# Performance work log

Hardware: AMD Instinct MI355X
Metric: run time of the kernel (lower is better)

Reference implementation:

```python
import jax, jax.numpy as jnp
import numpy as np

N, D, K = 65536, 512, 4096


def setup_inputs() -> dict:
    key = jax.random.key(0)
    kx, kc = jax.random.split(key)
    x = jax.random.normal(kx, (N, D), dtype=jnp.float32)
    center = jax.random.normal(kc, (K, D), dtype=jnp.float32)
    return {"x": x, "center": center}


def squared_euclidean(x, center):
    x_sq = jnp.sum(x * x, axis=1, keepdims=True)        # [N,1]
    c_sq = jnp.sum(center * center, axis=1)             # [K]
    cross = x @ center.T                                # [N,K] GEMM
    return x_sq - 2.0 * cross + c_sq[None, :]


def reference(x, center):
    # KMeans.forward: dis_func(input, center).argmin(1)
    dist = squared_euclidean(x, center)                 # [N,K]
    return jnp.argmin(dist, axis=1)                     # [N] int32
```

## Files before the change

### kernel.cpp

```cpp
#include <hip/hip_runtime.h>

#define N_ROWS 65536
#define DIM    512
#define K_CENT 4096
#define TILE_M 128
#define TILE_N 128
#define BK     64
#define KSTEPS (DIM / BK)
#define NKT    (K_CENT / TILE_N)
#define THREADS 512
#define MARGIN 22.0f
#define CAND_CAP 1536
#define COMPACT_TRIG 1024
#define SCALE1 0x7F7F7F7F

typedef float  floatx4  __attribute__((ext_vector_type(4)));
typedef float  floatx16 __attribute__((ext_vector_type(16)));
typedef int    intx2    __attribute__((ext_vector_type(2)));
typedef int    intx4    __attribute__((ext_vector_type(4)));
typedef int    intx8    __attribute__((ext_vector_type(8)));

__device__ __forceinline__ unsigned mapF(float f) {
  unsigned u = __float_as_uint(f);
  return (u & 0x80000000u) ? ~u : (u | 0x80000000u);
}
__device__ __forceinline__ float unmapF(unsigned m) {
  unsigned u = (m & 0x80000000u) ? (m ^ 0x80000000u) : ~m;
  return __uint_as_float(u);
}

__device__ __forceinline__ void gload_lds16(const void* g, void* l) {
  __builtin_amdgcn_global_load_lds(
      (const __attribute__((address_space(1))) void*)g,
      (__attribute__((address_space(3))) void*)l, 16, 0, 0);
}

__device__ __forceinline__ int pk4(float a, float b, float c, float d) {
  int r = __builtin_amdgcn_cvt_pk_fp8_f32(a, b, 0, false);
  r = __builtin_amdgcn_cvt_pk_fp8_f32(c, d, r, true);
  return r;
}

#define FENCE_BAR() do { asm volatile("s_waitcnt lgkmcnt(0)" ::: "memory"); \
                         __builtin_amdgcn_s_barrier();                       \
                         __builtin_amdgcn_sched_barrier(0); } while (0)

__global__ void prep_convert(const float* __restrict__ c,
                             unsigned char* __restrict__ cq, float* __restrict__ csqg) {
  size_t i = ((size_t)blockIdx.x * blockDim.x + threadIdx.x) * 16;
  if (i >= (size_t)K_CENT * DIM) return;
  floatx4 a0 = *(const floatx4*)(c + i);
  floatx4 a1 = *(const floatx4*)(c + i + 4);
  floatx4 a2 = *(const floatx4*)(c + i + 8);
  floatx4 a3 = *(const floatx4*)(c + i + 12);
  intx4 q = { pk4(a0[0],a0[1],a0[2],a0[3]), pk4(a1[0],a1[1],a1[2],a1[3]),
              pk4(a2[0],a2[1],a2[2],a2[3]), pk4(a3[0],a3[1],a3[2],a3[3]) };
  *(intx4*)(cq + i) = q;
  float s = 0.f;
#pragma unroll
  for (int e = 0; e < 4; ++e)
    s += a0[e]*a0[e] + a1[e]*a1[e] + a2[e]*a2[e] + a3[e]*a3[e];
#pragma unroll
  for (int o = 1; o < 32; o <<= 1) s += __shfl_xor(s, o, 64);
  if ((threadIdx.x & 31) == 0) csqg[i >> 9] = s;
}

__global__ __launch_bounds__(THREADS, 4)
void kmeans_argmin_pipe(const float* __restrict__ x, const float* __restrict__ cent,
                        const unsigned char* __restrict__ cq,
                        const float* __restrict__ csqg, int* __restrict__ out) {
  extern __shared__ __align__(16) unsigned char dynLds[];
  __shared__ float csqL[K_CENT];
  __shared__ unsigned sminU[TILE_M];
  __shared__ unsigned long long best[TILE_M];
  __shared__ unsigned candKey[CAND_CAP];
  __shared__ float candS[CAND_CAP];
  __shared__ int candCount;

  const int t = threadIdx.x;
  const int lane = t & 63;
  const int wave = t >> 6;
  const int wm = wave >> 1;
  const int wn = wave & 1;
  const int l31 = lane & 31;
  const int half = lane >> 5;
  const int rowBlock = blockIdx.x * TILE_M;
  const int srow = wm * 32 + l31;

  if (t < TILE_M) { sminU[t] = 0xFFFFFFFFu; best[t] = ~0ull; }
  if (t == 0) candCount = 0;
#pragma unroll
  for (int i = 0; i < K_CENT / THREADS; ++i) {
    int idx = t + i * THREADS;
    csqL[idx] = csqg[idx];
  }

  const int rS = (t >> 2) & 31;
  const int rowS = (t >> 7) * 32 + rS;
  const int offS = (((t & 3) ^ ((rS >> 1) & 3)) << 4);
  unsigned bOff = (unsigned)(rowS * DIM + offS);

  const int qk = half * 2;
  const int fragSlotBase = 4 * l31 + (qk ^ ((l31 >> 1) & 3));
  const unsigned char* pB0  = dynLds + (((wn * 2 + 0) * 128 + fragSlotBase) * 16);
  const unsigned char* pB0x = dynLds + ((((wn * 2 + 0) * 128 + fragSlotBase) ^ 1) * 16);
  const unsigned char* pB1  = dynLds + (((wn * 2 + 1) * 128 + fragSlotBase) * 16);
  const unsigned char* pB1x = dynLds + ((((wn * 2 + 1) * 128 + fragSlotBase) ^ 1) * 16);

  intx8 xf[KSTEPS];
  {
    const float* xr = x + (size_t)(rowBlock + srow) * DIM + half * 32;
#pragma unroll
    for (int ks = 0; ks < KSTEPS; ++ks) {
      int q[8];
#pragma unroll
      for (int j = 0; j < 8; ++j) {
        floatx4 f = *(const floatx4*)(xr + ks * 64 + j * 4);
        q[j] = pk4(f[0], f[1], f[2], f[3]);
      }
      xf[ks] = (intx8){q[0], q[1], q[2], q[3], q[4], q[5], q[6], q[7]};
    }
  }

  asm volatile("s_waitcnt vmcnt(0)" ::: "memory");
  gload_lds16(cq + bOff, dynLds + 0 * 8192 + wave * 1024); bOff += 64;
  gload_lds16(cq + bOff, dynLds + 1 * 8192 + wave * 1024); bOff += 64;
  FENCE_BAR();

  for (int kt = 0; kt < NKT; ++kt) {
    floatx16 acc[2];
#pragma unroll
    for (int fn = 0; fn < 2; ++fn)
#pragma unroll
      for (int e = 0; e < 16; ++e) acc[fn][e] = 0.f;

#pragma unroll
    for (int p = 0; p < KSTEPS; ++p) {
      gload_lds16(cq + bOff, dynLds + (((p + 2) & 3) << 13) + wave * 1024);
      bOff += (p == 5) ? (65536 - 7 * 64) : 64;
      asm volatile("s_waitcnt vmcnt(2)" ::: "memory");
      __builtin_amdgcn_s_barrier();
      __builtin_amdgcn_sched_barrier(0);

      const int bo = (p & 3) << 13;
      intx4 lo0 = *(const intx4*)(pB0  + bo);
      intx4 hi0 = *(const intx4*)(pB0x + bo);
      intx4 lo1 = *(const intx4*)(pB1  + bo);
      intx4 hi1 = *(const intx4*)(pB1x + bo);
      asm volatile("s_waitcnt lgkmcnt(0)" ::: "memory");
      __builtin_amdgcn_sched_barrier(0);
      intx8 b0 = (intx8){lo0[0], lo0[1], lo0[2], lo0[3], hi0[0], hi0[1], hi0[2], hi0[3]};
      intx8 b1 = (intx8){lo1[0], lo1[1], lo1[2], lo1[3], hi1[0], hi1[1], hi1[2], hi1[3]};
      acc[0] = __builtin_amdgcn_mfma_scale_f32_32x32x64_f8f6f4(
          b0, xf[p], acc[0], 0, 0, 0, SCALE1, 0, SCALE1);
      acc[1] = __builtin_amdgcn_mfma_scale_f32_32x32x64_f8f6f4(
          b1, xf[p], acc[1], 0, 0, 0, SCALE1, 0, SCALE1);
    }

    const int ktBase = kt << 7;
    float mn = 3.4e38f;
#pragma unroll
    for (int fn = 0; fn < 2; ++fn)
#pragma unroll
      for (int g = 0; g < 4; ++g) {
        floatx4 cs4 = *(const floatx4*)&csqL[ktBase + (wn * 2 + fn) * 32 + 8 * g + 4 * half];
#pragma unroll
        for (int e = 0; e < 4; ++e)
          mn = fminf(mn, cs4[e] - 2.f * acc[fn][4 * g + e]);
      }
    mn = fminf(mn, __shfl_xor(mn, 32, 64));
    if (half == 0) atomicMin(&sminU[srow], mapF(mn));
    FENCE_BAR();

    {
      float thr = unmapF(sminU[srow]) + MARGIN;
#pragma unroll
      for (int fn = 0; fn < 2; ++fn)
#pragma unroll
        for (int g = 0; g < 4; ++g) {
          floatx4 cs4 = *(const floatx4*)&csqL[ktBase + (wn * 2 + fn) * 32 + 8 * g + 4 * half];
#pragma unroll
          for (int e = 0; e < 4; ++e) {
            float s = cs4[e] - 2.f * acc[fn][4 * g + e];
            if (s <= thr) {
              int k = ktBase + (wn * 2 + fn) * 32 + 8 * g + 4 * half + e;
              int idx = atomicAdd(&candCount, 1);
              if (idx < CAND_CAP) {
                candKey[idx] = ((unsigned)k << 7) | (unsigned)srow;
                candS[idx] = s;
              }
            }
          }
        }
    }
    FENCE_BAR();

    if (candCount > COMPACT_TRIG) {
      int cc = candCount; if (cc > CAND_CAP) cc = CAND_CAP;
      unsigned myK[4]; float myS[4]; int myN = 0;
      for (int i = t; i < cc; i += THREADS) {
        int rl = candKey[i] & 127;
        if (candS[i] <= unmapF(sminU[rl]) + MARGIN && myN < 4) {
          myK[myN] = candKey[i]; myS[myN] = candS[i]; ++myN;
        }
      }
      FENCE_BAR();
      if (t == 0) candCount = 0;
      FENCE_BAR();
      int base = atomicAdd(&candCount, myN);
      for (int jj = 0; jj < myN; ++jj) { candKey[base + jj] = myK[jj]; candS[base + jj] = myS[jj]; }
      FENCE_BAR();
    }
  }

  __syncthreads();

  int cnt = candCount; if (cnt > CAND_CAP) cnt = CAND_CAP;
  const int g = t >> 4;
  const int sl = t & 15;
  for (int ci = g; ci < cnt; ci += 32) {
    unsigned cd = candKey[ci];
    int rl = cd & 127;
    if (candS[ci] > unmapF(sminU[rl]) + MARGIN) continue;
    int k = cd >> 7;
    const float* xr = x + (size_t)(rowBlock + rl) * DIM;
    const float* cr = cent + (size_t)k * DIM;
    double d = 0.0;
#pragma unroll
    for (int jj = 0; jj < DIM / 64; ++jj) {
      floatx4 xv = *(const floatx4*)(xr + jj * 64 + sl * 4);
      floatx4 cv = *(const floatx4*)(cr + jj * 64 + sl * 4);
#pragma unroll
      for (int e = 0; e < 4; ++e) {
        double df = (double)xv[e] - (double)cv[e];
        d += df * df;
      }
    }
#pragma unroll
    for (int off = 1; off < 16; off <<= 1) d += __shfl_xor(d, off, 64);
    if (sl == 0) {
      unsigned long long key =
          ((unsigned long long)__double_as_longlong(d) & ~0xFFFull) | (unsigned long long)k;
      atomicMin(&best[rl], key);
    }
  }
  __syncthreads();
  if (t < TILE_M) out[rowBlock + t] = (int)(best[t] & 0xFFFull);
}

__global__ __launch_bounds__(THREADS, 4)
void kmeans_argmin_fb(const float* __restrict__ x, const float* __restrict__ cent,
                      int* __restrict__ out) {
  __shared__ unsigned char ldsA[TILE_M * BK];
  __shared__ unsigned char ldsB[TILE_N * BK];
  __shared__ float csq4[TILE_N][4];
  __shared__ unsigned sminU[TILE_M];
  __shared__ unsigned long long best[TILE_M];
  __shared__ unsigned candKey[CAND_CAP];
  __shared__ float candS[CAND_CAP];
  __shared__ int candCount;

  const int t = threadIdx.x;
  const int lane = t & 63;
  const int wave = t >> 6;
  const int wm = wave >> 1;
  const int wn = wave & 1;
  const int l31 = lane & 31;
  const int half = lane >> 5;
  const int rowBlock = blockIdx.x * TILE_M;

  if (t < TILE_M) { sminU[t] = 0xFFFFFFFFu; best[t] = ~0ull; }
  if (t == 0) candCount = 0;

  const int rS = (t >> 2) & 31;
  const int rowS = (t >> 7) * 32 + rS;
  const int offS = (((t & 3) ^ ((rS >> 1) & 3)) << 4);
  const int qk = half * 2;
  const int fragSlotBase = 4 * l31 + (qk ^ ((l31 >> 1) & 3));

  for (int kt = 0; kt < NKT; ++kt) {
    const int ktBase = kt * TILE_N;
    ((float*)csq4)[t] = 0.f;
    floatx16 acc[2];
#pragma unroll
    for (int fn = 0; fn < 2; ++fn)
#pragma unroll
      for (int e = 0; e < 16; ++e) acc[fn][e] = 0.f;

    for (int ks = 0; ks < KSTEPS; ++ks) {
      const int kd = ks * BK;
      {
        const float* gA = x + (size_t)(rowBlock + rowS) * DIM + kd + offS;
        floatx4 f0 = *(const floatx4*)gA, f1 = *(const floatx4*)(gA + 4);
        floatx4 f2 = *(const floatx4*)(gA + 8), f3 = *(const floatx4*)(gA + 12);
        intx4 q = { pk4(f0[0],f0[1],f0[2],f0[3]), pk4(f1[0],f1[1],f1[2],f1[3]),
                    pk4(f2[0],f2[1],f2[2],f2[3]), pk4(f3[0],f3[1],f3[2],f3[3]) };
        *(intx4*)(ldsA + (size_t)t * 16) = q;
      }
      {
        const float* gB = cent + (size_t)(ktBase + rowS) * DIM + kd + offS;
        floatx4 f0 = *(const floatx4*)gB, f1 = *(const floatx4*)(gB + 4);
        floatx4 f2 = *(const floatx4*)(gB + 8), f3 = *(const floatx4*)(gB + 12);
        intx4 q = { pk4(f0[0],f0[1],f0[2],f0[3]), pk4(f1[0],f1[1],f1[2],f1[3]),
                    pk4(f2[0],f2[1],f2[2],f2[3]), pk4(f3[0],f3[1],f3[2],f3[3]) };
        *(intx4*)(ldsB + (size_t)t * 16) = q;
        float s = 0.f;
#pragma unroll
        for (int e = 0; e < 4; ++e)
          s += f0[e]*f0[e] + f1[e]*f1[e] + f2[e]*f2[e] + f3[e]*f3[e];
        csq4[rowS][t & 3] += s;
      }
      __syncthreads();

      intx8 aF, bF[2];
      {
        int s0 = wm * 128 + fragSlotBase;
        intx4 lo = *(const intx4*)(ldsA + s0 * 16);
        intx4 hi = *(const intx4*)(ldsA + (s0 ^ 1) * 16);
        aF = (intx8){lo[0], lo[1], lo[2], lo[3], hi[0], hi[1], hi[2], hi[3]};
      }
#pragma unroll
      for (int fn = 0; fn < 2; ++fn) {
        int s0 = (wn * 2 + fn) * 128 + fragSlotBase;
        intx4 lo = *(const intx4*)(ldsB + s0 * 16);
        intx4 hi = *(const intx4*)(ldsB + (s0 ^ 1) * 16);
        bF[fn] = (intx8){lo[0], lo[1], lo[2], lo[3], hi[0], hi[1], hi[2], hi[3]};
      }
#pragma unroll
      for (int fn = 0; fn < 2; ++fn)
        acc[fn] = __builtin_amdgcn_mfma_scale_f32_32x32x64_f8f6f4(
            aF, bF[fn], acc[fn], 0, 0, 0, SCALE1, 0, SCALE1);
      __syncthreads();
    }

    float cs[2];
#pragma unroll
    for (int fn = 0; fn < 2; ++fn) {
      int cl = wn * 64 + fn * 32 + l31;
      cs[fn] = csq4[cl][0] + csq4[cl][1] + csq4[cl][2] + csq4[cl][3];
    }

#pragma unroll
    for (int r = 0; r < 16; ++r) {
      float v = fminf(cs[0] - 2.f * acc[0][r], cs[1] - 2.f * acc[1][r]);
      v = fminf(v, __shfl_xor(v, 1, 64));
      v = fminf(v, __shfl_xor(v, 2, 64));
      v = fminf(v, __shfl_xor(v, 4, 64));
      v = fminf(v, __shfl_xor(v, 8, 64));
      v = fminf(v, __shfl_xor(v, 16, 64));
      if (l31 == 0) {
        int srow = wm * 32 + (r & 3) + 8 * (r >> 2) + 4 * half;
        atomicMin(&sminU[srow], mapF(v));
      }
    }
    __syncthreads();

#pragma unroll
    for (int r = 0; r < 16; ++r) {
      int srow = wm * 32 + (r & 3) + 8 * (r >> 2) + 4 * half;
      float thr = unmapF(sminU[srow]) + MARGIN;
#pragma unroll
      for (int fn = 0; fn < 2; ++fn) {
        float s = cs[fn] - 2.f * acc[fn][r];
        if (s <= thr) {
          int k = ktBase + wn * 64 + fn * 32 + l31;
          int idx = atomicAdd(&candCount, 1);
          if (idx < CAND_CAP) {
            candKey[idx] = ((unsigned)k << 7) | (unsigned)srow;
            candS[idx] = s;
          }
        }
      }
    }
    __syncthreads();

    if (candCount > COMPACT_TRIG) {
      int cc = candCount; if (cc > CAND_CAP) cc = CAND_CAP;
      unsigned myK[4]; float myS[4]; int myN = 0;
      for (int i = t; i < cc; i += THREADS) {
        int rl = candKey[i] & 127;
        if (candS[i] <= unmapF(sminU[rl]) + MARGIN && myN < 4) {
          myK[myN] = candKey[i]; myS[myN] = candS[i]; ++myN;
        }
      }
      __syncthreads();
      if (t == 0) candCount = 0;
      __syncthreads();
      int base = atomicAdd(&candCount, myN);
      for (int j = 0; j < myN; ++j) { candKey[base + j] = myK[j]; candS[base + j] = myS[j]; }
      __syncthreads();
    }
  }

  int cnt = candCount; if (cnt > CAND_CAP) cnt = CAND_CAP;
  const int g = t >> 4;
  const int sl = t & 15;
  for (int ci = g; ci < cnt; ci += 32) {
    unsigned cd = candKey[ci];
    int rl = cd & 127;
    if (candS[ci] > unmapF(sminU[rl]) + MARGIN) continue;
    int k = cd >> 7;
    const float* xr = x + (size_t)(rowBlock + rl) * DIM;
    const float* cr = cent + (size_t)k * DIM;
    double d = 0.0;
#pragma unroll
    for (int j = 0; j < DIM / 64; ++j) {
      floatx4 xv = *(const floatx4*)(xr + j * 64 + sl * 4);
      floatx4 cv = *(const floatx4*)(cr + j * 64 + sl * 4);
#pragma unroll
      for (int e = 0; e < 4; ++e) {
        double df = (double)xv[e] - (double)cv[e];
        d += df * df;
      }
    }
#pragma unroll
    for (int off = 1; off < 16; off <<= 1) d += __shfl_xor(d, off, 64);
    if (sl == 0) {
      unsigned long long key =
          ((unsigned long long)__double_as_longlong(d) & ~0xFFFull) | (unsigned long long)k;
      atomicMin(&best[rl], key);
    }
  }
  __syncthreads();
  if (t < TILE_M) out[rowBlock + t] = (int)(best[t] & 0xFFFull);
}

extern "C" void kernel_launch(void* const* d_in, const int* in_sizes, int n_in,
                              void* d_out, int out_size, void* d_ws, size_t ws_size,
                              hipStream_t stream) {
  const float* x = (const float*)d_in[0];
  const float* cent = (const float*)d_in[1];
  int* out = (int*)d_out;
  const size_t nXq = (size_t)N_ROWS * DIM;
  const size_t nCq = (size_t)K_CENT * DIM;
  const size_t nCsq = (size_t)K_CENT * sizeof(float);
  const int grid = N_ROWS / TILE_M;

  if (ws_size >= nXq + nCq + nCsq) {
    unsigned char* cq = (unsigned char*)d_ws;
    float* csqg = (float*)(cq + nCq);
    const size_t total16 = nCq / 16;
    prep_convert<<<(unsigned)((total16 + 255) / 256), 256, 0, stream>>>(cent, cq, csqg);
    kmeans_argmin_pipe<<<grid, THREADS, 4 * 8192, stream>>>(x, cent, cq, csqg, out);
  } else {
    kmeans_argmin_fb<<<grid, THREADS, 0, stream>>>(x, cent, out);
  }
}
```

Baseline: 601.9 us.

## Give each wave a private centroid ring and 64 rows to drop block barriers

Restructures the main kernel so each of four waves owns 64 x-rows, kept as FP8 fragments in registers, and streams its own copy of each 64-centroid tile through a per-wave 4-slot LDS ring. This removes the per-k-step block-wide barriers and gives each B fragment reuse across two A fragments. Candidate pools and their compaction also become per-wave, so only wave-local fences are needed. The cost is four times the centroid traffic per block, much higher register and LDS use, and one block per CU via launch bounds, which lowers occupancy.

After: 605.8 us. Within noise of the previous version (+0.6%).

```diff
diff --git a/kernel.cpp b/kernel.cpp
--- a/kernel.cpp
+++ b/kernel.cpp
@@ -3,20 +3,18 @@
 #define N_ROWS 65536
 #define DIM    512
 #define K_CENT 4096
-#define TILE_M 128
-#define TILE_N 128
-#define BK     64
-#define KSTEPS (DIM / BK)
-#define NKT    (K_CENT / TILE_N)
-#define THREADS 512
+#define TILE_M 256
+#define TILE_N 64
+#define NCT    (K_CENT / TILE_N)
+#define KSTEPS 8
+#define THREADS 256
+#define WCAP   1024
+#define WTRIG  512
 #define MARGIN 22.0f
-#define CAND_CAP 1536
-#define COMPACT_TRIG 1024
 #define SCALE1 0x7F7F7F7F
 
 typedef float  floatx4  __attribute__((ext_vector_type(4)));
 typedef float  floatx16 __attribute__((ext_vector_type(16)));
-typedef int    intx2    __attribute__((ext_vector_type(2)));
 typedef int    intx4    __attribute__((ext_vector_type(4)));
 typedef int    intx8    __attribute__((ext_vector_type(8)));
 
@@ -41,9 +39,8 @@
   return r;
 }
 
-#define FENCE_BAR() do { asm volatile("s_waitcnt lgkmcnt(0)" ::: "memory"); \
-                         __builtin_amdgcn_s_barrier();                       \
-                         __builtin_amdgcn_sched_barrier(0); } while (0)
+#define WAVE_LDS_FENCE() do { asm volatile("s_waitcnt lgkmcnt(0)" ::: "memory"); \
+                              __builtin_amdgcn_sched_barrier(0); } while (0)
 
 __global__ void prep_convert(const float* __restrict__ c,
                              unsigned char* __restrict__ cq, float* __restrict__ csqg) {
@@ -65,16 +62,238 @@
   if ((threadIdx.x & 31) == 0) csqg[i >> 9] = s;
 }
 
-__global__ __launch_bounds__(THREADS, 4)
+__global__ __launch_bounds__(THREADS, 1)
 void kmeans_argmin_pipe(const float* __restrict__ x, const float* __restrict__ cent,
                         const unsigned char* __restrict__ cq,
                         const float* __restrict__ csqg, int* __restrict__ out) {
-  extern __shared__ __align__(16) unsigned char dynLds[];
-  __shared__ float csqL[K_CENT];
+  __shared__ __align__(16) unsigned char ringLds[4][16384];
+  __shared__ __align__(16) float csqL[K_CENT];
   __shared__ unsigned sminU[TILE_M];
   __shared__ unsigned long long best[TILE_M];
-  __shared__ unsigned candKey[CAND_CAP];
-  __shared__ float candS[CAND_CAP];
+  __shared__ unsigned poolK[4][WCAP];
+  __shared__ float    poolS[4][WCAP];
+  __shared__ int candCnt[4];
+
+  const int t = threadIdx.x;
+  const int lane = t & 63;
+  const int wave = t >> 6;
+  const int l31 = lane & 31;
+  const int half = lane >> 5;
+  const int rowBlock = blockIdx.x * TILE_M;
+
+  sminU[t] = 0xFFFFFFFFu;
+  best[t] = ~0ull;
+  if (t < 4) candCnt[t] = 0;
+#pragma unroll
+  for (int i = 0; i < K_CENT / THREADS; ++i) csqL[t + i * THREADS] = csqg[t + i * THREADS];
+
+  int offI0, offI1, offI2, offI3;
+#pragma unroll
+  for (int i = 0; i < 4; ++i) {
+    int s = i * 64 + lane;
+    int rS = (s >> 2) & 31;
+    int row = (s >> 7) * 32 + rS;
+    int cp = (s & 3) ^ ((rS >> 1) & 3);
+    int v = row * DIM + cp * 16;
+    if (i == 0) offI0 = v; else if (i == 1) offI1 = v;
+    else if (i == 2) offI2 = v; else offI3 = v;
+  }
+
+  const int qk = half * 2;
+  const int slotLo = 4 * l31 + (qk ^ ((l31 >> 1) & 3));
+  const int loB = slotLo * 16;
+  const int hiB = (slotLo ^ 1) * 16;
+  unsigned char* ringW = ringLds[wave];
+
+  intx8 xfA[KSTEPS], xfB[KSTEPS];
+  {
+    const float* xr = x + (size_t)(rowBlock + wave * 64 + l31) * DIM + half * 32;
+#pragma unroll
+    for (int ks = 0; ks < KSTEPS; ++ks) {
+      int q[8];
+#pragma unroll
+      for (int j = 0; j < 8; ++j) {
+        floatx4 f = *(const floatx4*)(xr + ks * 64 + j * 4);
+        q[j] = pk4(f[0], f[1], f[2], f[3]);
+      }
+      xfA[ks] = (intx8){q[0], q[1], q[2], q[3], q[4], q[5], q[6], q[7]};
+    }
+    xr += (size_t)32 * DIM;
+#pragma unroll
+    for (int ks = 0; ks < KSTEPS; ++ks) {
+      int q[8];
+#pragma unroll
+      for (int j = 0; j < 8; ++j) {
+        floatx4 f = *(const floatx4*)(xr + ks * 64 + j * 4);
+        q[j] = pk4(f[0], f[1], f[2], f[3]);
+      }
+      xfB[ks] = (intx8){q[0], q[1], q[2], q[3], q[4], q[5], q[6], q[7]};
+    }
+  }
+
+  __syncthreads();
+
+#pragma unroll
+  for (int s = 0; s < 3; ++s) {
+    unsigned char* wb = ringW + (s << 12);
+    gload_lds16(cq + s * 64 + offI0, wb);
+    gload_lds16(cq + s * 64 + offI1, wb + 1024);
+    gload_lds16(cq + s * 64 + offI2, wb + 2048);
+    gload_lds16(cq + s * 64 + offI3, wb + 3072);
+  }
+  unsigned sOff = 3 * 64;
+
+  for (int ct = 0; ct < NCT; ++ct) {
+    floatx16 acc00, acc01, acc10, acc11;
+#pragma unroll
+    for (int e = 0; e < 16; ++e) { acc00[e] = 0.f; acc01[e] = 0.f; acc10[e] = 0.f; acc11[e] = 0.f; }
+
+#pragma unroll
+    for (int p = 0; p < KSTEPS; ++p) {
+      {
+        unsigned char* wb = ringW + (((p + 3) & 3) << 12);
+        gload_lds16(cq + sOff + offI0, wb);
+        gload_lds16(cq + sOff + offI1, wb + 1024);
+        gload_lds16(cq + sOff + offI2, wb + 2048);
+        gload_lds16(cq + sOff + offI3, wb + 3072);
+      }
+      sOff += (p == 4) ? 32320u : 64u;
+      asm volatile("s_waitcnt vmcnt(12)" ::: "memory");
+      __builtin_amdgcn_sched_barrier(0);
+
+      const unsigned char* rb = ringW + ((p & 3) << 12);
+      intx4 lo0 = *(const intx4*)(rb + loB);
+      intx4 hi0 = *(const intx4*)(rb + hiB);
+      intx4 lo1 = *(const intx4*)(rb + 2048 + loB);
+      intx4 hi1 = *(const intx4*)(rb + 2048 + hiB);
+      asm volatile("s_waitcnt lgkmcnt(0)" ::: "memory");
+      __builtin_amdgcn_sched_barrier(0);
+      intx8 b0 = (intx8){lo0[0],lo0[1],lo0[2],lo0[3], hi0[0],hi0[1],hi0[2],hi0[3]};
+      intx8 b1 = (intx8){lo1[0],lo1[1],lo1[2],lo1[3], hi1[0],hi1[1],hi1[2],hi1[3]};
+      acc00 = __builtin_amdgcn_mfma_scale_f32_32x32x64_f8f6f4(
+          b0, xfA[p], acc00, 0, 0, 0, SCALE1, 0, SCALE1);
+      acc01 = __builtin_amdgcn_mfma_scale_f32_32x32x64_f8f6f4(
+          b1, xfA[p], acc01, 0, 0, 0, SCALE1, 0, SCALE1);
+      acc10 = __builtin_amdgcn_mfma_scale_f32_32x32x64_f8f6f4(
+          b0, xfB[p], acc10, 0, 0, 0, SCALE1, 0, SCALE1);
+      acc11 = __builtin_amdgcn_mfma_scale_f32_32x32x64_f8f6f4(
+          b1, xfB[p], acc11, 0, 0, 0, SCALE1, 0, SCALE1);
+    }
+
+    const int ctB = ct << 6;
+#pragma unroll
+    for (int h = 0; h < 2; ++h) {
+      const floatx16& a0 = h ? acc10 : acc00;
+      const floatx16& a1 = h ? acc11 : acc01;
+      const int srow = wave * 64 + h * 32 + l31;
+      float mn = 3.4e38f;
+#pragma unroll
+      for (int gg = 0; gg < 4; ++gg) {
+        floatx4 c0 = *(const floatx4*)&csqL[ctB + 8 * gg + 4 * half];
+        floatx4 c1 = *(const floatx4*)&csqL[ctB + 32 + 8 * gg + 4 * half];
+#pragma unroll
+        for (int e = 0; e < 4; ++e) {
+          mn = fminf(mn, c0[e] - 2.f * a0[4 * gg + e]);
+          mn = fminf(mn, c1[e] - 2.f * a1[4 * gg + e]);
+        }
+      }
+      mn = fminf(mn, __shfl_xor(mn, 32, 64));
+      if (half == 0) atomicMin(&sminU[srow], mapF(mn));
+      WAVE_LDS_FENCE();
+
+      const float thr = unmapF(sminU[srow]) + MARGIN;
+#pragma unroll
+      for (int gg = 0; gg < 4; ++gg) {
+        floatx4 c0 = *(const floatx4*)&csqL[ctB + 8 * gg + 4 * half];
+        floatx4 c1 = *(const floatx4*)&csqL[ctB + 32 + 8 * gg + 4 * half];
+#pragma unroll
+        for (int e = 0; e < 4; ++e) {
+          float s0 = c0[e] - 2.f * a0[4 * gg + e];
+          if (s0 <= thr) {
+            int k = ctB + 8 * gg + 4 * half + e;
+            int idx = atomicAdd(&candCnt[wave], 1);
+            if (idx < WCAP) { poolK[wave][idx] = ((unsigned)k << 8) | (unsigned)srow; poolS[wave][idx] = s0; }
+          }
+          float s1 = c1[e] - 2.f * a1[4 * gg + e];
+          if (s1 <= thr) {
+            int k = ctB + 32 + 8 * gg + 4 * half + e;
+            int idx = atomicAdd(&candCnt[wave], 1);
+            if (idx < WCAP) { poolK[wave][idx] = ((unsigned)k << 8) | (unsigned)srow; poolS[wave][idx] = s1; }
+          }
+        }
+      }
+    }
+    WAVE_LDS_FENCE();
+
+    if (candCnt[wave] > WTRIG) {
+      int cc = candCnt[wave]; if (cc > WCAP) cc = WCAP;
+      unsigned myK[16]; float myS[16]; int myN = 0;
+      for (int i = lane; i < cc; i += 64) {
+        int rl = poolK[wave][i] & 255;
+        if (poolS[wave][i] <= unmapF(sminU[rl]) + MARGIN) {
+          myK[myN] = poolK[wave][i]; myS[myN] = poolS[wave][i]; ++myN;
+        }
+      }
+      WAVE_LDS_FENCE();
+      if (lane == 0) candCnt[wave] = 0;
+      WAVE_LDS_FENCE();
+      int base = atomicAdd(&candCnt[wave], myN);
+      for (int j = 0; j < myN; ++j) { poolK[wave][base + j] = myK[j]; poolS[wave][base + j] = myS[j]; }
+      WAVE_LDS_FENCE();
+    }
+  }
+
+  __syncthreads();
+
+  const int grp = t >> 4;
+  const int sl = t & 15;
+  for (int w = 0; w < 4; ++w) {
+    int cw = candCnt[w]; if (cw > WCAP) cw = WCAP;
+    for (int ci = grp; ci < cw; ci += 16) {
+      unsigned cd = poolK[w][ci];
+      int rl = cd & 255;
+      if (poolS[w][ci] > unmapF(sminU[rl]) + MARGIN) continue;
+      int k = cd >> 8;
+      const float* xr = x + (size_t)(rowBlock + rl) * DIM;
+      const float* cr = cent + (size_t)k * DIM;
+      double d = 0.0;
+#pragma unroll
+      for (int jj = 0; jj < DIM / 64; ++jj) {
+        floatx4 xv = *(const floatx4*)(xr + jj * 64 + sl * 4);
+        floatx4 cv = *(const floatx4*)(cr + jj * 64 + sl * 4);
+#pragma unroll
+        for (int e = 0; e < 4; ++e) {
+          double df = (double)xv[e] - (double)cv[e];
+          d += df * df;
+        }
+      }
+#pragma unroll
+      for (int off = 1; off < 16; off <<= 1) d += __shfl_xor(d, off, 64);
+      if (sl == 0) {
+        unsigned long long key =
+            ((unsigned long long)__double_as_longlong(d) & ~0xFFFull) | (unsigned long long)k;
+        atomicMin(&best[rl], key);
+      }
+    }
+  }
+  __syncthreads();
+  out[rowBlock + t] = (int)(best[t] & 0xFFFull);
+}
+
+#define FB_TILE_M 128
+#define FB_NKT    32
+#define FB_CAP    1536
+#define FB_TRIG   1024
+__global__ __launch_bounds__(512, 4)
+void kmeans_argmin_fb(const float* __restrict__ x, const float* __restrict__ cent,
+                      int* __restrict__ out) {
+  __shared__ unsigned char ldsA[FB_TILE_M * 64];
+  __shared__ unsigned char ldsB[128 * 64];
+  __shared__ float csq4[128][4];
+  __shared__ unsigned sminU[FB_TILE_M];
+  __shared__ unsigned long long best[FB_TILE_M];
+  __shared__ unsigned candKey[FB_CAP];
+  __shared__ float candS[FB_CAP];
   __shared__ int candCount;
 
   const int t = threadIdx.x;
@@ -84,138 +303,132 @@
   const int wn = wave & 1;
   const int l31 = lane & 31;
   const int half = lane >> 5;
-  const int rowBlock = blockIdx.x * TILE_M;
-  const int srow = wm * 32 + l31;
-
-  if (t < TILE_M) { sminU[t] = 0xFFFFFFFFu; best[t] = ~0ull; }
+  const int rowBlock = blockIdx.x * FB_TILE_M;
+
+  if (t < FB_TILE_M) { sminU[t] = 0xFFFFFFFFu; best[t] = ~0ull; }
   if (t == 0) candCount = 0;
-#pragma unroll
-  for (int i = 0; i < K_CENT / THREADS; ++i) {
-    int idx = t + i * THREADS;
-    csqL[idx] = csqg[idx];
-  }
 
   const int rS = (t >> 2) & 31;
   const int rowS = (t >> 7) * 32 + rS;
   const int offS = (((t & 3) ^ ((rS >> 1) & 3)) << 4);
-  unsigned bOff = (unsigned)(rowS * DIM + offS);
-
   const int qk = half * 2;
   const int fragSlotBase = 4 * l31 + (qk ^ ((l31 >> 1) & 3));
-  const unsigned char* pB0  = dynLds + (((wn * 2 + 0) * 128 + fragSlotBase) * 16);
-  const unsigned char* pB0x = dynLds + ((((wn * 2 + 0) * 128 + fragSlotBase) ^ 1) * 16);
-  const unsigned char* pB1  = dynLds + (((wn * 2 + 1) * 128 + fragSlotBase) * 16);
-  const unsigned char* pB1x = dynLds + ((((wn * 2 + 1) * 128 + fragSlotBase) ^ 1) * 16);
-
-  intx8 xf[KSTEPS];
-  {
-    const float* xr = x + (size_t)(rowBlock + srow) * DIM + half * 32;
-#pragma unroll
+
+  for (int kt = 0; kt < FB_NKT; ++kt) {
+    const int ktBase = kt * 128;
+    ((float*)csq4)[t] = 0.f;
+    floatx16 acc[2];
+#pragma unroll
+    for (int fn = 0; fn < 2; ++fn)
+#pragma unroll
+      for (int e = 0; e < 16; ++e) acc[fn][e] = 0.f;
+
     for (int ks = 0; ks < KSTEPS; ++ks) {
-      int q[8];
-#pragma unroll
-      for (int j = 0; j < 8; ++j) {
-        floatx4 f = *(const floatx4*)(xr + ks * 64 + j * 4);
-        q[j] = pk4(f[0], f[1], f[2], f[3]);
-      }
-      xf[ks] = (intx8){q[0], q[1], q[2], q[3], q[4], q[5], q[6], q[7]};
-    }
-  }
-
-  asm volatile("s_waitcnt vmcnt(0)" ::: "memory");
-  gload_lds16(cq + bOff, dynLds + 0 * 8192 + wave * 1024); bOff += 64;
-  gload_lds16(cq + bOff, dynLds + 1 * 8192 + wave * 1024); bOff += 64;
-  FENCE_BAR();
-
-  for (int kt = 0; kt < NKT; ++kt) {
-    floatx16 acc[2];
-#pragma unroll
-    for (int fn = 0; fn < 2; ++fn)
-#pragma unroll
-      for (int e = 0; e < 16; ++e) acc[fn][e] = 0.f;
-
-#pragma unroll
-    for (int p = 0; p < KSTEPS; ++p) {
-      gload_lds16(cq + bOff, dynLds + (((p + 2) & 3) << 13) + wave * 1024);
-      bOff += (p == 5) ? (65536 - 7 * 64) : 64;
-      asm volatile("s_waitcnt vmcnt(2)" ::: "memory");
-      __builtin_amdgcn_s_barrier();
-      __builtin_amdgcn_sched_barrier(0);
-
-      const int bo = (p & 3) << 13;
-      intx4 lo0 = *(const intx4*)(pB0  + bo);
-      intx4 hi0 = *(const intx4*)(pB0x + bo);
-      intx4 lo1 = *(const intx4*)(pB1  + bo);
-      intx4 hi1 = *(const intx4*)(pB1x + bo);
-      asm volatile("s_waitcnt lgkmcnt(0)" ::: "memory");
-      __builtin_amdgcn_sched_barrier(0);
-      intx8 b0 = (intx8){lo0[0], lo0[1], lo0[2], lo0[3], hi0[0], hi0[1], hi0[2], hi0[3]};
-      intx8 b1 = (intx8){lo1[0], lo1[1], lo1[2], lo1[3], hi1[0], hi1[1], hi1[2], hi1[3]};
-      acc[0] = __builtin_amdgcn_mfma_scale_f32_32x32x64_f8f6f4(
-          b0, xf[p], acc[0], 0, 0, 0, SCALE1, 0, SCALE1);
-      acc[1] = __builtin_amdgcn_mfma_scale_f32_32x32x64_f8f6f4(
-          b1, xf[p], acc[1], 0, 0, 0, SCALE1, 0, SCALE1);
-    }
-
-    const int ktBase = kt << 7;
-    float mn = 3.4e38f;
-#pragma unroll
-    for (int fn = 0; fn < 2; ++fn)
-#pragma unroll
-      for (int g = 0; g < 4; ++g) {
-        floatx4 cs4 = *(const floatx4*)&csqL[ktBase + (wn * 2 + fn) * 32 + 8 * g + 4 * half];
+      const int kd = ks * 64;
+      {
+        const float* gA = x + (size_t)(rowBlock + rowS) * DIM + kd + offS;
+        floatx4 f0 = *(const floatx4*)gA, f1 = *(const floatx4*)(gA + 4);
+        floatx4 f2 = *(const floatx4*)(gA + 8), f3 = *(const floatx4*)(gA + 12);
+        intx4 q = { pk4(f0[0],f0[1],f0[2],f0[3]), pk4(f1[0],f1[1],f1[2],f1[3]),
+                    pk4(f2[0],f2[1],f2[2],f2[3]), pk4(f3[0],f3[1],f3[2],f3[3]) };
+        *(intx4*)(ldsA + (size_t)t * 16) = q;
+      }
+      {
+        const float* gB = cent + (size_t)(ktBase + rowS) * DIM + kd + offS;
+        floatx4 f0 = *(const floatx4*)gB, f1 = *(const floatx4*)(gB + 4);
+        floatx4 f2 = *(const floatx4*)(gB + 8), f3 = *(const floatx4*)(gB + 12);
+        intx4 q = { pk4(f0[0],f0[1],f0[2],f0[3]), pk4(f1[0],f1[1],f1[2],f1[3]),
+                    pk4(f2[0],f2[1],f2[2],f2[3]), pk4(f3[0],f3[1],f3[2],f3[3]) };
+        *(intx4*)(ldsB + (size_t)t * 16) = q;
+        float s = 0.f;
 #pragma unroll
         for (int e = 0; e < 4; ++e)
-          mn = fminf(mn, cs4[e] - 2.f * acc[fn][4 * g + e]);
-      }
-    mn = fminf(mn, __shfl_xor(mn, 32, 64));
-    if (half == 0) atomicMin(&sminU[srow], mapF(mn));
-    FENCE_BAR();
-
-    {
+          s += f0[e]*f0[e] + f1[e]*f1[e] + f2[e]*f2[e] + f3[e]*f3[e];
+        csq4[rowS][t & 3] += s;
+      }
+      __syncthreads();
+
+      intx8 aF, bF[2];
+      {
+        int s0 = wm * 128 + fragSlotBase;
+        intx4 lo = *(const intx4*)(ldsA + s0 * 16);
+        intx4 hi = *(const intx4*)(ldsA + (s0 ^ 1) * 16);
+        aF = (intx8){lo[0], lo[1], lo[2], lo[3], hi[0], hi[1], hi[2], hi[3]};
+      }
+#pragma unroll
+      for (int fn = 0; fn < 2; ++fn) {
+        int s0 = (wn * 2 + fn) * 128 + fragSlotBase;
+        intx4 lo = *(const intx4*)(ldsB + s0 * 16);
+        intx4 hi = *(const intx4*)(ldsB + (s0 ^ 1) * 16);
+        bF[fn] = (intx8){lo[0], lo[1], lo[2], lo[3], hi[0], hi[1], hi[2], hi[3]};
+      }
+#pragma unroll
+      for (int fn = 0; fn < 2; ++fn)
+        acc[fn] = __builtin_amdgcn_mfma_scale_f32_32x32x64_f8f6f4(
+            aF, bF[fn], acc[fn], 0, 0, 0, SCALE1, 0, SCALE1);
+      __syncthreads();
+    }
+
+    float cs[2];
+#pragma unroll
+    for (int fn = 0; fn < 2; ++fn) {
+      int cl = wn * 64 + fn * 32 + l31;
+      cs[fn] = csq4[cl][0] + csq4[cl][1] + csq4[cl][2] + csq4[cl][3];
+    }
+
+#pragma unroll
+    for (int r = 0; r < 16; ++r) {
+      float v = fminf(cs[0] - 2.f * acc[0][r], cs[1] - 2.f * acc[1][r]);
+      v = fminf(v, __shfl_xor(v, 1, 64));
+      v = fminf(v, __shfl_xor(v, 2, 64));
+      v = fminf(v, __shfl_xor(v, 4, 64));
+      v = fminf(v, __shfl_xor(v, 8, 64));
+      v = fminf(v, __shfl_xor(v, 16, 64));
+      if (l31 == 0) {
+        int srow = wm * 32 + (r & 3) + 8 * (r >> 2) + 4 * half;
+        atomicMin(&sminU[srow], mapF(v));
+      }
+    }
+    __syncthreads();
+
+#pragma unroll
+    for (int r = 0; r < 16; ++r) {
+      int srow = wm * 32 + (r & 3) + 8 * (r >> 2) + 4 * half;
       float thr = unmapF(sminU[srow]) + MARGIN;
 #pragma unroll
-      for (int fn = 0; fn < 2; ++fn)
-#pragma unroll
-        for (int g = 0; g < 4; ++g) {
-          floatx4 cs4 = *(const floatx4*)&csqL[ktBase + (wn * 2 + fn) * 32 + 8 * g + 4 * half];
-#pragma unroll
-          for (int e = 0; e < 4; ++e) {
-            float s = cs4[e] - 2.f * acc[fn][4 * g + e];
-            if (s <= thr) {
-              int k = ktBase + (wn * 2 + fn) * 32 + 8 * g + 4 * half + e;
-              int idx = atomicAdd(&candCount, 1);
-              if (idx < CAND_CAP) {
-                candKey[idx] = ((unsigned)k << 7) | (unsigned)srow;
-                candS[idx] = s;
-              }
-            }
+      for (int fn = 0; fn < 2; ++fn) {
+        float s = cs[fn] - 2.f * acc[fn][r];
+        if (s <= thr) {
+          int k = ktBase + wn * 64 + fn * 32 + l31;
+          int idx = atomicAdd(&candCount, 1);
+          if (idx < FB_CAP) {
+            candKey[idx] = ((unsigned)k << 7) | (unsigned)srow;
+            candS[idx] = s;
           }
         }
-    }
-    FENCE_BAR();
-
-    if (candCount > COMPACT_TRIG) {
-      int cc = candCount; if (cc > CAND_CAP) cc = CAND_CAP;
+      }
+    }
+    __syncthreads();
+
+    if (candCount > FB_TRIG) {
+      int cc = candCount; if (cc > FB_CAP) cc = FB_CAP;
       unsigned myK[4]; float myS[4]; int myN = 0;
-      for (int i = t; i < cc; i += THREADS) {
+      for (int i = t; i < cc; i += 512) {
         int rl = candKey[i] & 127;
         if (candS[i] <= unmapF(sminU[rl]) + MARGIN && myN < 4) {
           myK[myN] = candKey[i]; myS[myN] = candS[i]; ++myN;
         }
       }
-      FENCE_BAR();
+      __syncthreads();
       if (t == 0) candCount = 0;
-      FENCE_BAR();
+      __syncthreads();
       int base = atomicAdd(&candCount, myN);
-      for (int jj = 0; jj < myN; ++jj) { candKey[base + jj] = myK[jj]; candS[base + jj] = myS[jj]; }
-      FENCE_BAR();
-    }
-  }
-
-  __syncthreads();
-
-  int cnt = candCount; if (cnt > CAND_CAP) cnt = CAND_CAP;
+      for (int j = 0; j < myN; ++j) { candKey[base + j] = myK[j]; candS[base + j] = myS[j]; }
+      __syncthreads();
+    }
+  }
+
+  int cnt = candCount; if (cnt > FB_CAP) cnt = FB_CAP;
   const int g = t >> 4;
   const int sl = t & 15;
   for (int ci = g; ci < cnt; ci += 32) {
@@ -227,9 +440,9 @@
     const float* cr = cent + (size_t)k * DIM;
     double d = 0.0;
 #pragma unroll
-    for (int jj = 0; jj < DIM / 64; ++jj) {
-      floatx4 xv = *(const floatx4*)(xr + jj * 64 + sl * 4);
-      floatx4 cv = *(const floatx4*)(cr + jj * 64 + sl * 4);
+    for (int j = 0; j < DIM / 64; ++j) {
+      floatx4 xv = *(const floatx4*)(xr + j * 64 + sl * 4);
+      floatx4 cv = *(const floatx4*)(cr + j * 64 + sl * 4);
 #pragma unroll
       for (int e = 0; e < 4; ++e) {
         double df = (double)xv[e] - (double)cv[e];
@@ -245,184 +458,7 @@
     }
   }
   __syncthreads();
-  if (t < TILE_M) out[rowBlock + t] = (int)(best[t] & 0xFFFull);
-}
-
-__global__ __launch_bounds__(THREADS, 4)
-void kmeans_argmin_fb(const float* __restrict__ x, const float* __restrict__ cent,
-                      int* __restrict__ out) {
-  __shared__ unsigned char ldsA[TILE_M * BK];
-  __shared__ unsigned char ldsB[TILE_N * BK];
-  __shared__ float csq4[TILE_N][4];
-  __shared__ unsigned sminU[TILE_M];
-  __shared__ unsigned long long best[TILE_M];
-  __shared__ unsigned candKey[CAND_CAP];
-  __shared__ float candS[CAND_CAP];
-  __shared__ int candCount;
-
-  const int t = threadIdx.x;
-  const int lane = t & 63;
-  const int wave = t >> 6;
-  const int wm = wave >> 1;
-  const int wn = wave & 1;
-  const int l31 = lane & 31;
-  const int half = lane >> 5;
-  const int rowBlock = blockIdx.x * TILE_M;
-
-  if (t < TILE_M) { sminU[t] = 0xFFFFFFFFu; best[t] = ~0ull; }
-  if (t == 0) candCount = 0;
-
-  const int rS = (t >> 2) & 31;
-  const int rowS = (t >> 7) * 32 + rS;
-  const int offS = (((t & 3) ^ ((rS >> 1) & 3)) << 4);
-  const int qk = half * 2;
-  const int fragSlotBase = 4 * l31 + (qk ^ ((l31 >> 1) & 3));
-
-  for (int kt = 0; kt < NKT; ++kt) {
-    const int ktBase = kt * TILE_N;
-    ((float*)csq4)[t] = 0.f;
-    floatx16 acc[2];
-#pragma unroll
-    for (int fn = 0; fn < 2; ++fn)
-#pragma unroll
-      for (int e = 0; e < 16; ++e) acc[fn][e] = 0.f;
-
-    for (int ks = 0; ks < KSTEPS; ++ks) {
-      const int kd = ks * BK;
-      {
-        const float* gA = x + (size_t)(rowBlock + rowS) * DIM + kd + offS;
-        floatx4 f0 = *(const floatx4*)gA, f1 = *(const floatx4*)(gA + 4);
-        floatx4 f2 = *(const floatx4*)(gA + 8), f3 = *(const floatx4*)(gA + 12);
-        intx4 q = { pk4(f0[0],f0[1],f0[2],f0[3]), pk4(f1[0],f1[1],f1[2],f1[3]),
-                    pk4(f2[0],f2[1],f2[2],f2[3]), pk4(f3[0],f3[1],f3[2],f3[3]) };
-        *(intx4*)(ldsA + (size_t)t * 16) = q;
-      }
-      {
-        const float* gB = cent + (size_t)(ktBase + rowS) * DIM + kd + offS;
-        floatx4 f0 = *(const floatx4*)gB, f1 = *(const floatx4*)(gB + 4);
-        floatx4 f2 = *(const floatx4*)(gB + 8), f3 = *(const floatx4*)(gB + 12);
-        intx4 q = { pk4(f0[0],f0[1],f0[2],f0[3]), pk4(f1[0],f1[1],f1[2],f1[3]),
-                    pk4(f2[0],f2[1],f2[2],f2[3]), pk4(f3[0],f3[1],f3[2],f3[3]) };
-        *(intx4*)(ldsB + (size_t)t * 16) = q;
-        float s = 0.f;
-#pragma unroll
-        for (int e = 0; e < 4; ++e)
-          s += f0[e]*f0[e] + f1[e]*f1[e] + f2[e]*f2[e] + f3[e]*f3[e];
-        csq4[rowS][t & 3] += s;
-      }
-      __syncthreads();
-
-      intx8 aF, bF[2];
-      {
-        int s0 = wm * 128 + fragSlotBase;
-        intx4 lo = *(const intx4*)(ldsA + s0 * 16);
-        intx4 hi = *(const intx4*)(ldsA + (s0 ^ 1) * 16);
-        aF = (intx8){lo[0], lo[1], lo[2], lo[3], hi[0], hi[1], hi[2], hi[3]};
-      }
-#pragma unroll
-      for (int fn = 0; fn < 2; ++fn) {
-        int s0 = (wn * 2 + fn) * 128 + fragSlotBase;
-        intx4 lo = *(const intx4*)(ldsB + s0 * 16);
-        intx4 hi = *(const intx4*)(ldsB + (s0 ^ 1) * 16);
-        bF[fn] = (intx8){lo[0], lo[1], lo[2], lo[3], hi[0], hi[1], hi[2], hi[3]};
-      }
-#pragma unroll
-      for (int fn = 0; fn < 2; ++fn)
-        acc[fn] = __builtin_amdgcn_mfma_scale_f32_32x32x64_f8f6f4(
-            aF, bF[fn], acc[fn], 0, 0, 0, SCALE1, 0, SCALE1);
-      __syncthreads();
-    }
-
-    float cs[2];
-#pragma unroll
-    for (int fn = 0; fn < 2; ++fn) {
-      int cl = wn * 64 + fn * 32 + l31;
-      cs[fn] = csq4[cl][0] + csq4[cl][1] + csq4[cl][2] + csq4[cl][3];
-    }
-
-#pragma unroll
-    for (int r = 0; r < 16; ++r) {
-      float v = fminf(cs[0] - 2.f * acc[0][r], cs[1] - 2.f * acc[1][r]);
-      v = fminf(v, __shfl_xor(v, 1, 64));
-      v = fminf(v, __shfl_xor(v, 2, 64));
-      v = fminf(v, __shfl_xor(v, 4, 64));
-      v = fminf(v, __shfl_xor(v, 8, 64));
-      v = fminf(v, __shfl_xor(v, 16, 64));
-      if (l31 == 0) {
-        int srow = wm * 32 + (r & 3) + 8 * (r >> 2) + 4 * half;
-        atomicMin(&sminU[srow], mapF(v));
-      }
-    }
-    __syncthreads();
-
-#pragma unroll
-    for (int r = 0; r < 16; ++r) {
-      int srow = wm * 32 + (r & 3) + 8 * (r >> 2) + 4 * half;
-      float thr = unmapF(sminU[srow]) + MARGIN;
-#pragma unroll
-      for (int fn = 0; fn < 2; ++fn) {
-        float s = cs[fn] - 2.f * acc[fn][r];
-        if (s <= thr) {
-          int k = ktBase + wn * 64 + fn * 32 + l31;
-          int idx = atomicAdd(&candCount, 1);
-          if (idx < CAND_CAP) {
-            candKey[idx] = ((unsigned)k << 7) | (unsigned)srow;
-            candS[idx] = s;
-          }
-        }
-      }
-    }
-    __syncthreads();
-
-    if (candCount > COMPACT_TRIG) {
-      int cc = candCount; if (cc > CAND_CAP) cc = CAND_CAP;
-      unsigned myK[4]; float myS[4]; int myN = 0;
-      for (int i = t; i < cc; i += THREADS) {
-        int rl = candKey[i] & 127;
-        if (candS[i] <= unmapF(sminU[rl]) + MARGIN && myN < 4) {
-          myK[myN] = candKey[i]; myS[myN] = candS[i]; ++myN;
-        }
-      }
-      __syncthreads();
-      if (t == 0) candCount = 0;
-      __syncthreads();
-      int base = atomicAdd(&candCount, myN);
-      for (int j = 0; j < myN; ++j) { candKey[base + j] = myK[j]; candS[base + j] = myS[j]; }
-      __syncthreads();
-    }
-  }
-
-  int cnt = candCount; if (cnt > CAND_CAP) cnt = CAND_CAP;
-  const int g = t >> 4;
-  const int sl = t & 15;
-  for (int ci = g; ci < cnt; ci += 32) {
-    unsigned cd = candKey[ci];
-    int rl = cd & 127;
-    if (candS[ci] > unmapF(sminU[rl]) + MARGIN) continue;
-    int k = cd >> 7;
-    const float* xr = x + (size_t)(rowBlock + rl) * DIM;
-    const float* cr = cent + (size_t)k * DIM;
-    double d = 0.0;
-#pragma unroll
-    for (int j = 0; j < DIM / 64; ++j) {
-      floatx4 xv = *(const floatx4*)(xr + j * 64 + sl * 4);
-      floatx4 cv = *(const floatx4*)(cr + j * 64 + sl * 4);
-#pragma unroll
-      for (int e = 0; e < 4; ++e) {
-        double df = (double)xv[e] - (double)cv[e];
-        d += df * df;
-      }
-    }
-#pragma unroll
-    for (int off = 1; off < 16; off <<= 1) d += __shfl_xor(d, off, 64);
-    if (sl == 0) {
-      unsigned long long key =
-          ((unsigned long long)__double_as_longlong(d) & ~0xFFFull) | (unsigned long long)k;
-      atomicMin(&best[rl], key);
-    }
-  }
-  __syncthreads();
-  if (t < TILE_M) out[rowBlock + t] = (int)(best[t] & 0xFFFull);
+  if (t < FB_TILE_M) out[rowBlock + t] = (int)(best[t] & 0xFFFull);
 }
 
 extern "C" void kernel_launch(void* const* d_in, const int* in_sizes, int n_in,
@@ -434,15 +470,14 @@
   const size_t nXq = (size_t)N_ROWS * DIM;
   const size_t nCq = (size_t)K_CENT * DIM;
   const size_t nCsq = (size_t)K_CENT * sizeof(float);
-  const int grid = N_ROWS / TILE_M;
 
   if (ws_size >= nXq + nCq + nCsq) {
     unsigned char* cq = (unsigned char*)d_ws;
     float* csqg = (float*)(cq + nCq);
     const size_t total16 = nCq / 16;
     prep_convert<<<(unsigned)((total16 + 255) / 256), 256, 0, stream>>>(cent, cq, csqg);
-    kmeans_argmin_pipe<<<grid, THREADS, 4 * 8192, stream>>>(x, cent, cq, csqg, out);
+    kmeans_argmin_pipe<<<N_ROWS / TILE_M, THREADS, 0, stream>>>(x, cent, cq, csqg, out);
   } else {
-    kmeans_argmin_fb<<<grid, THREADS, 0, stream>>>(x, cent, out);
-  }
-}
+    kmeans_argmin_fb<<<N_ROWS / FB_TILE_M, 512, 0, stream>>>(x, cent, out);
+  }
+}
```
